# Kernel optimization log

Measured on AMD Instinct MI355X. Metric: run time of the kernel, lower is better.

## Reference

```python
import jax, jax.numpy as jnp
import numpy as np

B, S, D = 2, 2048, 1024
H, DH = 16, 64  # n_heads, d_head; inner_dim = H*DH = 1024


def setup_inputs() -> dict:
    key = jax.random.key(0)
    ks = jax.random.split(key, 6)
    s = 0.02
    return {
        "query": jax.random.normal(ks[0], (B, S, D), jnp.float32),
        "context": jax.random.normal(ks[1], (B, S, D), jnp.float32),
        "Wq": jax.random.normal(ks[2], (D, H * DH), jnp.float32) * s,
        "Wk": jax.random.normal(ks[3], (D, H * DH), jnp.float32) * s,
        "Wv": jax.random.normal(ks[4], (D, H * DH), jnp.float32) * s,
        "Wo": jax.random.normal(ks[5], (H * DH, D), jnp.float32) * s,
        "bo": jnp.zeros((D,), jnp.float32),
    }


def reference(query, context, Wq, Wk, Wv, Wo, bo):
    scale = DH ** -0.5
    # projections -> [B, H, S, DH]
    q = (query @ Wq).reshape(B, S, H, DH).transpose(0, 2, 1, 3)
    k = (context @ Wk).reshape(B, S, H, DH).transpose(0, 2, 1, 3)
    v = (context @ Wv).reshape(B, S, H, DH).transpose(0, 2, 1, 3)
    scores = jnp.einsum("bhqd,bhkd->bhqk", q, k) * scale  # [B,H,S,S]
    probs = jax.nn.softmax(scores, axis=-1)
    out = jnp.einsum("bhqk,bhkd->bhqd", probs, v)  # [B,H,S,DH]
    out = out.transpose(0, 2, 1, 3).reshape(B, S, H * DH)
    return out @ Wo + bo
```

## Files before the change

kernel.cpp:

```cpp
#include <hip/hip_runtime.h>
#include <hip/hip_bf16.h>

typedef __attribute__((ext_vector_type(8))) short bf16x8;
typedef __attribute__((ext_vector_type(4))) float f32x4;
typedef __attribute__((ext_vector_type(16))) float f32x16;

#define B_ 2
#define S_ 2048
#define D_ 1024
#define H_ 16

__device__ __forceinline__ unsigned short f2bf(float x) {
  unsigned u = __float_as_uint(x);
  unsigned r = (u + 0x7fffu + ((u >> 16) & 1u)) >> 16;
  return (unsigned short)r;
}

__device__ __forceinline__ float bf2f(unsigned short x) {
  return __uint_as_float((unsigned)x << 16);
}

__device__ __forceinline__ unsigned cvt_pk_bf16(float lo, float hi) {
  unsigned r;
  asm("v_cvt_pk_bf16_f32 %0, %1, %2" : "=v"(r) : "v"(lo), "v"(hi));
  return r;
}

__device__ __forceinline__ void gload_lds16(const void* g, void* l) {
  __builtin_amdgcn_global_load_lds((const __attribute__((address_space(1))) void*)g,
                                   (__attribute__((address_space(3))) void*)l, 16, 0, 0);
}

#define VM_BARRIER(N) do {                                   \
    asm volatile("s_waitcnt vmcnt(" #N ")" ::: "memory");    \
    __builtin_amdgcn_s_barrier();                            \
    __builtin_amdgcn_sched_barrier(0);                       \
  } while (0)

__global__ __launch_bounds__(256) void prep_kernel(const float* __restrict__ query,
                                                   const float* __restrict__ ctx,
                                                   const float* __restrict__ Wq, const float* __restrict__ Wk,
                                                   const float* __restrict__ Wv, const float* __restrict__ Wo,
                                                   unsigned short* __restrict__ qb, unsigned short* __restrict__ cb,
                                                   unsigned short* __restrict__ WqT, unsigned short* __restrict__ WkT,
                                                   unsigned short* __restrict__ WvT, unsigned short* __restrict__ WoT) {
  __shared__ float tile[32][33];
  int bid = blockIdx.x;
  if (bid < 8192) {
    const float* s = bid < 4096 ? query : ctx;
    unsigned short* d = bid < 4096 ? qb : cb;
    int i = (bid & 4095) * 256 + threadIdx.x;
    float4 v = ((const float4*)s)[i];
    ushort4 o;
    o.x = f2bf(v.x); o.y = f2bf(v.y); o.z = f2bf(v.z); o.w = f2bf(v.w);
    ((ushort4*)d)[i] = o;
    return;
  }
  int tid = bid - 8192;
  int z = tid >> 10, r = tid & 1023;
  const float* W; unsigned short* WT;
  if (z == 0)      { W = Wq; WT = WqT; }
  else if (z == 1) { W = Wk; WT = WkT; }
  else if (z == 2) { W = Wv; WT = WvT; }
  else             { W = Wo; WT = WoT; }
  int r0 = (r >> 5) * 32, c0 = (r & 31) * 32;
  int t = threadIdx.x;
  int lr = t >> 3, lc = (t & 7) * 4;
  float4 v = *(const float4*)&W[(size_t)(r0 + lr) * 1024 + c0 + lc];
  tile[lr][lc + 0] = v.x; tile[lr][lc + 1] = v.y; tile[lr][lc + 2] = v.z; tile[lr][lc + 3] = v.w;
  __syncthreads();
  ushort4 o;
  o.x = f2bf(tile[lc + 0][lr]);
  o.y = f2bf(tile[lc + 1][lr]);
  o.z = f2bf(tile[lc + 2][lr]);
  o.w = f2bf(tile[lc + 3][lr]);
  *(ushort4*)&WT[(size_t)(c0 + lr) * 1024 + r0 + lc] = o;
}

template<int BM, int BN>
__device__ __forceinline__ void gemm_core(const unsigned short* __restrict__ A,
                                          const unsigned short* __restrict__ BT,
                                          int m0, int n0,
                                          unsigned short* As, unsigned short* Bs,
                                          f32x4 (&acc)[BM / 32][BN / 32]) {
  const int t = threadIdx.x, w = t >> 6, l = t & 63;
  const int lr = l & 15, lg = (l >> 4) * 8;
  const int wm = (w >> 1) * (BM / 2), wn = (w & 1) * (BN / 2);
  constexpr int K = 1024;
  constexpr int AI = BM / 64, BI = BN / 64, NLD = AI + BI;

#define GSTAGE(buf, k0) do {                                                               \
    _Pragma("unroll")                                                                      \
    for (int it_ = 0; it_ < AI; ++it_) {                                                   \
      int o_ = t * 16 + it_ * 4096;                                                        \
      int row_ = o_ >> 6, ce_ = (o_ & 63) >> 1;                                            \
      gload_lds16(A + (size_t)(m0 + row_) * K + (k0) + ce_,                                \
                  (char*)As + (buf) * (BM * 64) + it_ * 4096 + w * 1024);                  \
    }                                                                                      \
    _Pragma("unroll")                                                                      \
    for (int it_ = 0; it_ < BI; ++it_) {                                                   \
      int o_ = t * 16 + it_ * 4096;                                                        \
      int row_ = o_ >> 6, ce_ = (o_ & 63) >> 1;                                            \
      gload_lds16(BT + (size_t)(n0 + row_) * K + (k0) + ce_,                               \
                  (char*)Bs + (buf) * (BN * 64) + it_ * 4096 + w * 1024);                  \
    }                                                                                      \
  } while (0)

  GSTAGE(0, 0);
  GSTAGE(1, 32);
  if constexpr (NLD == 4) VM_BARRIER(4); else VM_BARRIER(3);
  int cur = 0;
  for (int kt = 0; kt < 32; ++kt) {
    int nb = cur + 2; if (nb >= 3) nb -= 3;
    if (kt < 30) GSTAGE(nb, (kt + 2) * 32);
    bf16x8 af[BM / 32], bfr[BN / 32];
#pragma unroll
    for (int mi = 0; mi < BM / 32; ++mi)
      af[mi] = *(const bf16x8*)&As[cur * (BM * 32) + (wm + mi * 16 + lr) * 32 + lg];
#pragma unroll
    for (int ni = 0; ni < BN / 32; ++ni)
      bfr[ni] = *(const bf16x8*)&Bs[cur * (BN * 32) + (wn + ni * 16 + lr) * 32 + lg];
    __builtin_amdgcn_s_setprio(1);
#pragma unroll
    for (int mi = 0; mi < BM / 32; ++mi)
#pragma unroll
      for (int ni = 0; ni < BN / 32; ++ni)
        acc[mi][ni] = __builtin_amdgcn_mfma_f32_16x16x32_bf16(af[mi], bfr[ni], acc[mi][ni], 0, 0, 0);
    __builtin_amdgcn_s_setprio(0);
    if (kt < 30) { if constexpr (NLD == 4) VM_BARRIER(4); else VM_BARRIER(3); }
    else if (kt == 30) VM_BARRIER(0);
    cur = (cur == 2) ? 0 : cur + 1;
  }
#undef GSTAGE
}

__global__ __launch_bounds__(256) void gemm_qkv(const unsigned short* __restrict__ qb,
                                                const unsigned short* __restrict__ cb,
                                                const unsigned short* __restrict__ WqT,
                                                const unsigned short* __restrict__ WkT,
                                                const unsigned short* __restrict__ WvT,
                                                unsigned short* __restrict__ qp,
                                                unsigned short* __restrict__ kp,
                                                unsigned short* __restrict__ vt) {
  __shared__ unsigned short As[3 * 4096];
  __shared__ unsigned short Bs[3 * 4096];
  int wg = (blockIdx.x & 7) * 96 + (blockIdx.x >> 3);
  int z = wg >> 8, r = wg & 255;
  const unsigned short *A, *BT; unsigned short* C; int N, bx, by;
  float osc;
  if (z == 0)      { A = qb;  BT = WqT; C = qp; N = 1024; bx = r & 31; by = r >> 5; osc = 0.125f * 1.44269504089f; }
  else if (z == 1) { A = cb;  BT = WkT; C = kp; N = 1024; bx = r & 31; by = r >> 5; osc = 1.f; }
  else             { A = WvT; BT = cb;  C = vt; N = 4096; bx = r & 7;  by = r >> 3; osc = 1.f; }
  f32x4 acc[4][4];
#pragma unroll
  for (int mi = 0; mi < 4; ++mi)
#pragma unroll
    for (int ni = 0; ni < 4; ++ni) acc[mi][ni] = {0.f, 0.f, 0.f, 0.f};
  gemm_core<128, 128>(A, BT, bx * 128, by * 128, As, Bs, acc);
  const int t = threadIdx.x, w = t >> 6, l = t & 63;
  const int lr = l & 15, lg4 = (l >> 4) * 4;
  const int wm = (w >> 1) * 64, wn = (w & 1) * 64;
#pragma unroll
  for (int mi = 0; mi < 4; ++mi)
#pragma unroll
    for (int ni = 0; ni < 4; ++ni)
#pragma unroll
      for (int j = 0; j < 4; ++j)
        C[(size_t)(bx * 128 + wm + mi * 16 + lg4 + j) * N + by * 128 + wn + ni * 16 + lr] =
            f2bf(acc[mi][ni][j] * osc);
}

__global__ __launch_bounds__(256) void gemm_out(const unsigned short* __restrict__ A,
                                                const unsigned short* __restrict__ BT,
                                                const float* __restrict__ bias,
                                                float* __restrict__ C) {
  __shared__ unsigned short As[3 * 4096];
  __shared__ unsigned short Bs[3 * 2048];
  int wg = (blockIdx.x & 7) * 64 + (blockIdx.x >> 3);
  int by = wg & 15, bx = wg >> 4;
  f32x4 acc[4][2];
#pragma unroll
  for (int mi = 0; mi < 4; ++mi)
#pragma unroll
    for (int ni = 0; ni < 2; ++ni) acc[mi][ni] = {0.f, 0.f, 0.f, 0.f};
  gemm_core<128, 64>(A, BT, bx * 128, by * 64, As, Bs, acc);
  const int t = threadIdx.x, w = t >> 6, l = t & 63;
  const int lr = l & 15, lg4 = (l >> 4) * 4;
  const int wm = (w >> 1) * 64, wn = (w & 1) * 32;
#pragma unroll
  for (int mi = 0; mi < 4; ++mi)
#pragma unroll
    for (int ni = 0; ni < 2; ++ni) {
      int col = by * 64 + wn + ni * 16 + lr;
      float bv = bias[col];
#pragma unroll
      for (int j = 0; j < 4; ++j)
        C[(size_t)(bx * 128 + wm + mi * 16 + lg4 + j) * 1024 + col] = acc[mi][ni][j] + bv;
    }
}

__global__ __launch_bounds__(256, 4) void attn_kernel(const unsigned short* __restrict__ Q,
                                                      const unsigned short* __restrict__ Kp,
                                                      const unsigned short* __restrict__ Vt,
                                                      unsigned short* __restrict__ Op0,
                                                      unsigned short* __restrict__ Op1,
                                                      float* __restrict__ Lp) {
  __shared__ char lds[32768];
  const int t = threadIdx.x, w = t >> 6, l = t & 63;
  const int l31 = l & 31, hi = l >> 5;
  const int u = (blockIdx.x & 7) * 128 + (blockIdx.x >> 3);
  const int half = u >> 9, nf = u & 511;
  const int qt = nf & 15, h = (nf >> 4) & 15, b = nf >> 8;

  const int q = qt * 128 + w * 32 + l31;
  const size_t qbase = ((size_t)(b * S_ + q)) * 1024 + h * 64;
  bf16x8 qf[4];
#pragma unroll
  for (int c = 0; c < 4; ++c) qf[c] = *(const bf16x8*)&Q[qbase + c * 16 + hi * 8];

  union { unsigned short s[8]; bf16x8 v; } ones;
#pragma unroll
  for (int i = 0; i < 8; ++i) ones.s[i] = 0x3F80;

  const size_t kbase = (size_t)b * S_ * 1024 + h * 64 + ((size_t)half << 20);
  const size_t vtb = (size_t)(h * 64) * 4096 + (size_t)b * 2048 + half * 1024;

  f32x16 oacc[2];
  f32x16 lacc;
#pragma unroll
  for (int r = 0; r < 16; ++r) { oacc[0][r] = 0.f; oacc[1][r] = 0.f; lacc[r] = 0.f; }

#define STAGE(bsel, kv0) do {                                                          \
    char* kdst = lds + (bsel) * 16384;                                                 \
    char* vdst = kdst + 8192;                                                          \
    _Pragma("unroll")                                                                  \
    for (int it_ = 0; it_ < 2; ++it_) {                                                \
      const int off_ = it_ * 4096 + w * 1024 + l * 16;                                 \
      const int row_ = off_ >> 7, cb_ = off_ & 127;                                    \
      const int sc_ = (cb_ ^ ((row_ & 7) << 4)) >> 1;                                  \
      gload_lds16(Kp + kbase + (size_t)((kv0) + row_) * 1024 + sc_,                    \
                  kdst + it_ * 4096 + w * 1024);                                       \
      gload_lds16(Vt + vtb + (size_t)row_ * 4096 + (kv0) + sc_,                        \
                  vdst + it_ * 4096 + w * 1024);                                       \
    }                                                                                  \
  } while (0)

  STAGE(0, 0);
  VM_BARRIER(0);
  int cur = 0;
  const int sw = (l & 7) << 4;

  for (int tile = 0; tile < 16; ++tile) {
    if (tile < 15) STAGE(cur ^ 1, (tile + 1) * 64);
    const char* kb = lds + cur * 16384;
    const char* vb = kb + 8192;

#pragma unroll
    for (int kvb = 0; kvb < 2; ++kvb) {
      f32x16 sacc;
#pragma unroll
      for (int r = 0; r < 16; ++r) sacc[r] = 0.f;
      const int row = kvb * 32 + l31;
      __builtin_amdgcn_s_setprio(1);
#pragma unroll
      for (int c = 0; c < 4; ++c) {
        bf16x8 kf = *(const bf16x8*)(kb + row * 128 + ((c * 32 + hi * 16) ^ sw));
        sacc = __builtin_amdgcn_mfma_f32_32x32x16_bf16(kf, qf[c], sacc, 0, 0, 0);
      }
      __builtin_amdgcn_s_setprio(0);

#pragma unroll
      for (int r = 0; r < 16; ++r) sacc[r] = __builtin_amdgcn_exp2f(sacc[r]);

#pragma unroll
      for (int ch = 0; ch < 2; ++ch) {
        const int c = kvb * 2 + ch, r0 = ch * 8;
        unsigned wA = cvt_pk_bf16(sacc[r0 + 0], sacc[r0 + 1]);
        unsigned wB = cvt_pk_bf16(sacc[r0 + 2], sacc[r0 + 3]);
        unsigned wC = cvt_pk_bf16(sacc[r0 + 4], sacc[r0 + 5]);
        unsigned wD = cvt_pk_bf16(sacc[r0 + 6], sacc[r0 + 7]);
        asm("v_permlane32_swap_b32 %0, %1" : "+v"(wA), "+v"(wC));
        asm("v_permlane32_swap_b32 %0, %1" : "+v"(wB), "+v"(wD));
        union { unsigned u[4]; bf16x8 v; } pf;
        pf.u[0] = wA; pf.u[1] = wB; pf.u[2] = wC; pf.u[3] = wD;
        __builtin_amdgcn_s_setprio(1);
#pragma unroll
        for (int d = 0; d < 2; ++d) {
          const int vrow = d * 32 + l31;
          bf16x8 vf = *(const bf16x8*)(vb + vrow * 128 + ((c * 32 + hi * 16) ^ sw));
          oacc[d] = __builtin_amdgcn_mfma_f32_32x32x16_bf16(vf, pf.v, oacc[d], 0, 0, 0);
        }
        lacc = __builtin_amdgcn_mfma_f32_32x32x16_bf16(ones.v, pf.v, lacc, 0, 0, 0);
        __builtin_amdgcn_s_setprio(0);
      }
    }
    if (tile < 15) VM_BARRIER(0);
    cur ^= 1;
  }

  unsigned short* Op = half ? Op1 : Op0;
#pragma unroll
  for (int d = 0; d < 2; ++d)
#pragma unroll
    for (int rg = 0; rg < 4; ++rg) {
      ushort4 o4;
      o4.x = f2bf(oacc[d][rg * 4 + 0]);
      o4.y = f2bf(oacc[d][rg * 4 + 1]);
      o4.z = f2bf(oacc[d][rg * 4 + 2]);
      o4.w = f2bf(oacc[d][rg * 4 + 3]);
      *(ushort4*)&Op[qbase + d * 32 + rg * 8 + hi * 4] = o4;
    }
  if (!hi) Lp[half * 65536 + (b * 16 + h) * 2048 + q] = lacc[0];
#undef STAGE
}

__global__ __launch_bounds__(256) void combine_kernel(unsigned short* __restrict__ Op0,
                                                      const unsigned short* __restrict__ Op1,
                                                      const float* __restrict__ Lp) {
  int e8 = blockIdx.x * 256 + threadIdx.x;
  int r = e8 >> 7, c = (e8 & 127) * 8;
  int b = r >> 11, s = r & 2047, h = c >> 6;
  float la = Lp[(b * 16 + h) * 2048 + s];
  float lb = Lp[65536 + (b * 16 + h) * 2048 + s];
  float inv = 1.f / (la + lb);
  size_t off = (size_t)r * 1024 + c;
  ushort4 a0 = *(ushort4*)&Op0[off], a1 = *(ushort4*)&Op0[off + 4];
  ushort4 b0 = *(const ushort4*)&Op1[off], b1 = *(const ushort4*)&Op1[off + 4];
  ushort4 o0, o1;
  o0.x = f2bf((bf2f(a0.x) + bf2f(b0.x)) * inv);
  o0.y = f2bf((bf2f(a0.y) + bf2f(b0.y)) * inv);
  o0.z = f2bf((bf2f(a0.z) + bf2f(b0.z)) * inv);
  o0.w = f2bf((bf2f(a0.w) + bf2f(b0.w)) * inv);
  o1.x = f2bf((bf2f(a1.x) + bf2f(b1.x)) * inv);
  o1.y = f2bf((bf2f(a1.y) + bf2f(b1.y)) * inv);
  o1.z = f2bf((bf2f(a1.z) + bf2f(b1.z)) * inv);
  o1.w = f2bf((bf2f(a1.w) + bf2f(b1.w)) * inv);
  *(ushort4*)&Op0[off] = o0;
  *(ushort4*)&Op0[off + 4] = o1;
}

extern "C" void kernel_launch(void* const* d_in, const int* in_sizes, int n_in,
                              void* d_out, int out_size, void* d_ws, size_t ws_size,
                              hipStream_t stream) {
  const float* query   = (const float*)d_in[0];
  const float* context = (const float*)d_in[1];
  const float* Wq = (const float*)d_in[2];
  const float* Wk = (const float*)d_in[3];
  const float* Wv = (const float*)d_in[4];
  const float* Wo = (const float*)d_in[5];
  const float* bo = (const float*)d_in[6];
  float* out = (float*)d_out;

  const size_t NA = (size_t)B_ * S_ * D_;
  const size_t NW = (size_t)D_ * D_;
  unsigned short* ws  = (unsigned short*)d_ws;
  unsigned short* qb  = ws;
  unsigned short* cb  = qb + NA;
  unsigned short* WqT = cb + NA;
  unsigned short* WkT = WqT + NW;
  unsigned short* WvT = WkT + NW;
  unsigned short* WoT = WvT + NW;
  unsigned short* qp  = WoT + NW;
  unsigned short* kp  = qp + NA;
  unsigned short* vt  = kp + NA;
  unsigned short* Op0 = qb;
  unsigned short* Op1 = cb;
  float* Lp = (float*)WqT;
  unsigned short* ao  = qb;

  prep_kernel<<<12288, 256, 0, stream>>>(query, context, Wq, Wk, Wv, Wo,
                                         qb, cb, WqT, WkT, WvT, WoT);
  gemm_qkv<<<768, 256, 0, stream>>>(qb, cb, WqT, WkT, WvT, qp, kp, vt);
  attn_kernel<<<1024, 256, 0, stream>>>(qp, kp, vt, Op0, Op1, Lp);
  combine_kernel<<<2048, 256, 0, stream>>>(Op0, Op1, Lp);
  gemm_out<<<512, 256, 0, stream>>>(ao, WoT, bo, out);
}
```

Measured before the change: 121.7 us.

## Load V fragments directly from global and triple-buffer K tiles in LDS

Stops staging V tiles through LDS. Each wave now reads its V^T fragments straight from global memory into registers inside the PV loop. Only K is staged through LDS, now as a three-buffer ring prefetched two tiles ahead with a partial vmcnt wait. This cuts LDS use from 32 KB to 24 KB and removes the LDS write/read traffic for V, but all four waves now fetch the same V data redundantly and wait on global-load latency directly in the inner loop.

```diff
diff --git a/kernel.cpp b/kernel.cpp
--- a/kernel.cpp
+++ b/kernel.cpp
@@ -205,7 +205,7 @@
                                                       unsigned short* __restrict__ Op0,
                                                       unsigned short* __restrict__ Op1,
                                                       float* __restrict__ Lp) {
-  __shared__ char lds[32768];
+  __shared__ char lds[24576];
   const int t = threadIdx.x, w = t >> 6, l = t & 63;
   const int l31 = l & 31, hi = l >> 5;
   const int u = (blockIdx.x & 7) * 128 + (blockIdx.x >> 3);
@@ -224,15 +224,16 @@
 
   const size_t kbase = (size_t)b * S_ * 1024 + h * 64 + ((size_t)half << 20);
   const size_t vtb = (size_t)(h * 64) * 4096 + (size_t)b * 2048 + half * 1024;
+  const unsigned short* vp0 = Vt + vtb + (size_t)l31 * 4096 + hi * 8;
+  const unsigned short* vp1 = vp0 + (size_t)32 * 4096;
 
   f32x16 oacc[2];
   f32x16 lacc;
 #pragma unroll
   for (int r = 0; r < 16; ++r) { oacc[0][r] = 0.f; oacc[1][r] = 0.f; lacc[r] = 0.f; }
 
-#define STAGE(bsel, kv0) do {                                                          \
-    char* kdst = lds + (bsel) * 16384;                                                 \
-    char* vdst = kdst + 8192;                                                          \
+#define KSTAGE(bsel, kv0) do {                                                         \
+    char* kdst = lds + (bsel) * 8192;                                                  \
     _Pragma("unroll")                                                                  \
     for (int it_ = 0; it_ < 2; ++it_) {                                                \
       const int off_ = it_ * 4096 + w * 1024 + l * 16;                                 \
@@ -240,20 +241,20 @@
       const int sc_ = (cb_ ^ ((row_ & 7) << 4)) >> 1;                                  \
       gload_lds16(Kp + kbase + (size_t)((kv0) + row_) * 1024 + sc_,                    \
                   kdst + it_ * 4096 + w * 1024);                                       \
-      gload_lds16(Vt + vtb + (size_t)row_ * 4096 + (kv0) + sc_,                        \
-                  vdst + it_ * 4096 + w * 1024);                                       \
     }                                                                                  \
   } while (0)
 
-  STAGE(0, 0);
-  VM_BARRIER(0);
+  KSTAGE(0, 0);
+  KSTAGE(1, 64);
+  VM_BARRIER(2);
   int cur = 0;
   const int sw = (l & 7) << 4;
 
   for (int tile = 0; tile < 16; ++tile) {
-    if (tile < 15) STAGE(cur ^ 1, (tile + 1) * 64);
-    const char* kb = lds + cur * 16384;
-    const char* vb = kb + 8192;
+    if (tile < 14) { int nb = cur + 2; if (nb >= 3) nb -= 3; KSTAGE(nb, (tile + 2) * 64); }
+    const char* kb = lds + cur * 8192;
+    const unsigned short* vt0 = vp0 + tile * 64;
+    const unsigned short* vt1 = vp1 + tile * 64;
 
 #pragma unroll
     for (int kvb = 0; kvb < 2; ++kvb) {
@@ -275,6 +276,8 @@
 #pragma unroll
       for (int ch = 0; ch < 2; ++ch) {
         const int c = kvb * 2 + ch, r0 = ch * 8;
+        bf16x8 vf0 = *(const bf16x8*)(vt0 + c * 16);
+        bf16x8 vf1 = *(const bf16x8*)(vt1 + c * 16);
         unsigned wA = cvt_pk_bf16(sacc[r0 + 0], sacc[r0 + 1]);
         unsigned wB = cvt_pk_bf16(sacc[r0 + 2], sacc[r0 + 3]);
         unsigned wC = cvt_pk_bf16(sacc[r0 + 4], sacc[r0 + 5]);
@@ -284,18 +287,15 @@
         union { unsigned u[4]; bf16x8 v; } pf;
         pf.u[0] = wA; pf.u[1] = wB; pf.u[2] = wC; pf.u[3] = wD;
         __builtin_amdgcn_s_setprio(1);
-#pragma unroll
-        for (int d = 0; d < 2; ++d) {
-          const int vrow = d * 32 + l31;
-          bf16x8 vf = *(const bf16x8*)(vb + vrow * 128 + ((c * 32 + hi * 16) ^ sw));
-          oacc[d] = __builtin_amdgcn_mfma_f32_32x32x16_bf16(vf, pf.v, oacc[d], 0, 0, 0);
-        }
+        oacc[0] = __builtin_amdgcn_mfma_f32_32x32x16_bf16(vf0, pf.v, oacc[0], 0, 0, 0);
+        oacc[1] = __builtin_amdgcn_mfma_f32_32x32x16_bf16(vf1, pf.v, oacc[1], 0, 0, 0);
         lacc = __builtin_amdgcn_mfma_f32_32x32x16_bf16(ones.v, pf.v, lacc, 0, 0, 0);
         __builtin_amdgcn_s_setprio(0);
       }
     }
-    if (tile < 15) VM_BARRIER(0);
-    cur ^= 1;
+    if (tile < 14) VM_BARRIER(2);
+    else if (tile == 14) VM_BARRIER(0);
+    cur = (cur == 2) ? 0 : cur + 1;
   }
 
   unsigned short* Op = half ? Op1 : Op0;
@@ -311,7 +311,7 @@
       *(ushort4*)&Op[qbase + d * 32 + rg * 8 + hi * 4] = o4;
     }
   if (!hi) Lp[half * 65536 + (b * 16 + h) * 2048 + q] = lacc[0];
-#undef STAGE
+#undef KSTAGE
 }
 
 __global__ __launch_bounds__(256) void combine_kernel(unsigned short* __restrict__ Op0,
```

Result: slower. 149.1 us (+22.6%).

## Interleave QK MFMAs for both KV halves and overlap exp with PV MFMAs

Applied to the files above, without the earlier changes.

Restructures the attention inner loop so that the QK^T MFMAs for both 32-row KV sub-blocks are issued together, and the exp2 of the second block is interleaved between the PV MFMA groups of the first. The aim is to hide transcendental (exp) latency and MFMA dependency stalls behind independent matrix work. It costs more live VGPRs, since two score accumulators are held at once, which could reduce occupancy or cause spills.

```diff
diff --git a/kernel.cpp b/kernel.cpp
--- a/kernel.cpp
+++ b/kernel.cpp
@@ -245,55 +245,73 @@
     }                                                                                  \
   } while (0)
 
+#define PACK(sv, r0, pf) do {                                                          \
+    unsigned a_ = cvt_pk_bf16(sv[(r0) + 0], sv[(r0) + 1]);                             \
+    unsigned b_ = cvt_pk_bf16(sv[(r0) + 2], sv[(r0) + 3]);                             \
+    unsigned c_ = cvt_pk_bf16(sv[(r0) + 4], sv[(r0) + 5]);                             \
+    unsigned d_ = cvt_pk_bf16(sv[(r0) + 6], sv[(r0) + 7]);                             \
+    asm("v_permlane32_swap_b32 %0, %1" : "+v"(a_), "+v"(c_));                          \
+    asm("v_permlane32_swap_b32 %0, %1" : "+v"(b_), "+v"(d_));                          \
+    pf.u[0] = a_; pf.u[1] = b_; pf.u[2] = c_; pf.u[3] = d_;                            \
+  } while (0)
+
+#define PV(cc, pf) do {                                                                \
+    bf16x8 vf0_ = *(const bf16x8*)(vb + l31 * 128 + (((cc) * 32 + hi * 16) ^ sw));     \
+    bf16x8 vf1_ = *(const bf16x8*)(vb + (32 + l31) * 128 + (((cc) * 32 + hi * 16) ^ sw)); \
+    oacc[0] = __builtin_amdgcn_mfma_f32_32x32x16_bf16(vf0_, pf.v, oacc[0], 0, 0, 0);   \
+    oacc[1] = __builtin_amdgcn_mfma_f32_32x32x16_bf16(vf1_, pf.v, oacc[1], 0, 0, 0);   \
+    lacc = __builtin_amdgcn_mfma_f32_32x32x16_bf16(ones.v, pf.v, lacc, 0, 0, 0);       \
+  } while (0)
+
   STAGE(0, 0);
   VM_BARRIER(0);
   int cur = 0;
   const int sw = (l & 7) << 4;
+  union PFU { unsigned u[4]; bf16x8 v; };
 
   for (int tile = 0; tile < 16; ++tile) {
     if (tile < 15) STAGE(cur ^ 1, (tile + 1) * 64);
     const char* kb = lds + cur * 16384;
     const char* vb = kb + 8192;
 
-#pragma unroll
-    for (int kvb = 0; kvb < 2; ++kvb) {
-      f32x16 sacc;
-#pragma unroll
-      for (int r = 0; r < 16; ++r) sacc[r] = 0.f;
-      const int row = kvb * 32 + l31;
-      __builtin_amdgcn_s_setprio(1);
-#pragma unroll
-      for (int c = 0; c < 4; ++c) {
-        bf16x8 kf = *(const bf16x8*)(kb + row * 128 + ((c * 32 + hi * 16) ^ sw));
-        sacc = __builtin_amdgcn_mfma_f32_32x32x16_bf16(kf, qf[c], sacc, 0, 0, 0);
-      }
-      __builtin_amdgcn_s_setprio(0);
-
-#pragma unroll
-      for (int r = 0; r < 16; ++r) sacc[r] = __builtin_amdgcn_exp2f(sacc[r]);
-
-#pragma unroll
-      for (int ch = 0; ch < 2; ++ch) {
-        const int c = kvb * 2 + ch, r0 = ch * 8;
-        unsigned wA = cvt_pk_bf16(sacc[r0 + 0], sacc[r0 + 1]);
-        unsigned wB = cvt_pk_bf16(sacc[r0 + 2], sacc[r0 + 3]);
-        unsigned wC = cvt_pk_bf16(sacc[r0 + 4], sacc[r0 + 5]);
-        unsigned wD = cvt_pk_bf16(sacc[r0 + 6], sacc[r0 + 7]);
-        asm("v_permlane32_swap_b32 %0, %1" : "+v"(wA), "+v"(wC));
-        asm("v_permlane32_swap_b32 %0, %1" : "+v"(wB), "+v"(wD));
-        union { unsigned u[4]; bf16x8 v; } pf;
-        pf.u[0] = wA; pf.u[1] = wB; pf.u[2] = wC; pf.u[3] = wD;
-        __builtin_amdgcn_s_setprio(1);
-#pragma unroll
-        for (int d = 0; d < 2; ++d) {
-          const int vrow = d * 32 + l31;
-          bf16x8 vf = *(const bf16x8*)(vb + vrow * 128 + ((c * 32 + hi * 16) ^ sw));
-          oacc[d] = __builtin_amdgcn_mfma_f32_32x32x16_bf16(vf, pf.v, oacc[d], 0, 0, 0);
-        }
-        lacc = __builtin_amdgcn_mfma_f32_32x32x16_bf16(ones.v, pf.v, lacc, 0, 0, 0);
-        __builtin_amdgcn_s_setprio(0);
-      }
+    f32x16 s0, s1;
+#pragma unroll
+    for (int r = 0; r < 16; ++r) { s0[r] = 0.f; s1[r] = 0.f; }
+    __builtin_amdgcn_s_setprio(1);
+#pragma unroll
+    for (int c = 0; c < 4; ++c) {
+      bf16x8 kf0 = *(const bf16x8*)(kb + l31 * 128 + ((c * 32 + hi * 16) ^ sw));
+      bf16x8 kf1 = *(const bf16x8*)(kb + (32 + l31) * 128 + ((c * 32 + hi * 16) ^ sw));
+      s0 = __builtin_amdgcn_mfma_f32_32x32x16_bf16(kf0, qf[c], s0, 0, 0, 0);
+      s1 = __builtin_amdgcn_mfma_f32_32x32x16_bf16(kf1, qf[c], s1, 0, 0, 0);
     }
+    __builtin_amdgcn_s_setprio(0);
+
+#pragma unroll
+    for (int r = 0; r < 16; ++r) s0[r] = __builtin_amdgcn_exp2f(s0[r]);
+
+    PFU pf;
+    PACK(s0, 0, pf);
+    __builtin_amdgcn_s_setprio(1);
+    PV(0, pf);
+    __builtin_amdgcn_s_setprio(0);
+#pragma unroll
+    for (int r = 0; r < 8; ++r) s1[r] = __builtin_amdgcn_exp2f(s1[r]);
+    PACK(s0, 8, pf);
+    __builtin_amdgcn_s_setprio(1);
+    PV(1, pf);
+    __builtin_amdgcn_s_setprio(0);
+#pragma unroll
+    for (int r = 8; r < 16; ++r) s1[r] = __builtin_amdgcn_exp2f(s1[r]);
+    PACK(s1, 0, pf);
+    __builtin_amdgcn_s_setprio(1);
+    PV(2, pf);
+    __builtin_amdgcn_s_setprio(0);
+    PACK(s1, 8, pf);
+    __builtin_amdgcn_s_setprio(1);
+    PV(3, pf);
+    __builtin_amdgcn_s_setprio(0);
+
     if (tile < 15) VM_BARRIER(0);
     cur ^= 1;
   }
@@ -312,6 +330,8 @@
     }
   if (!hi) Lp[half * 65536 + (b * 16 + h) * 2048 + q] = lacc[0];
 #undef STAGE
+#undef PACK
+#undef PV
 }
 
 __global__ __launch_bounds__(256) void combine_kernel(unsigned short* __restrict__ Op0,
```

Result: no change. 123.4 us (+1.4%).
